# Performance work log

Measured on AMD Instinct MI355X. Metric: run time of the kernel, lower is better.

Reference implementation:

```python
import jax, jax.numpy as jnp
import numpy as np

N_EMBD = 1024
N_HEAD = 16
HEAD_DIM = N_EMBD // N_HEAD


def setup_inputs() -> dict:
    key = jax.random.key(0)
    ks = jax.random.split(key, 5)
    B, S = 2, 2048
    scale = 0.02
    return {
        "hidden_states": jax.random.normal(ks[0], (B, S, N_EMBD), dtype=jnp.float32),
        "w_attn": jax.random.normal(ks[1], (N_EMBD, 3 * N_EMBD), dtype=jnp.float32) * scale,
        "b_attn": jnp.zeros((3 * N_EMBD,), dtype=jnp.float32),
        "w_proj": jax.random.normal(ks[2], (N_EMBD, N_EMBD), dtype=jnp.float32) * scale,
        "b_proj": jnp.zeros((N_EMBD,), dtype=jnp.float32),
    }


def reference(hidden_states, w_attn, b_attn, w_proj, b_proj):
    B, S, _ = hidden_states.shape
    qkv = hidden_states @ w_attn + b_attn                     # [B,S,3E]
    q, k, v = jnp.split(qkv, 3, axis=-1)                      # each [B,S,E]

    def split_heads(t):  # [B,S,E] -> [B,H,S,D]
        return t.reshape(B, S, N_HEAD, HEAD_DIM).transpose(0, 2, 1, 3)

    q, k, v = split_heads(q), split_heads(k), split_heads(v)

    scores = jnp.einsum("bhqd,bhkd->bhqk", q, k) / np.sqrt(HEAD_DIM).astype(np.float32)
    causal = jnp.tril(jnp.ones((S, S), dtype=bool))
    scores = jnp.where(causal[None, None], scores, jnp.float32(-jnp.inf))
    attn = jax.nn.softmax(scores, axis=-1)                    # [B,H,S,S]
    out = jnp.einsum("bhqk,bhkd->bhqd", attn, v)              # [B,H,S,D]
    out = out.transpose(0, 2, 1, 3).reshape(B, S, N_EMBD)     # merge heads
    out = out @ w_proj + b_proj
    return out
```

## Files before the change

kernel.cpp:

```cpp
#include <hip/hip_runtime.h>
#include <hip/hip_bf16.h>


typedef __attribute__((ext_vector_type(4))) float  float4v;
typedef __attribute__((ext_vector_type(8))) short  short8v;
typedef __attribute__((ext_vector_type(4))) short  short4v;

#define ATT_SCALE 0.18033688011112042f

__device__ __forceinline__ short f2bf(float f) {
  union { float f; unsigned u; } v; v.f = f;
  unsigned r = v.u + 0x7fffu + ((v.u >> 16) & 1u);
  return (short)(r >> 16);
}
__device__ __forceinline__ float bf2f(short s) {
  union { unsigned u; float f; } v; v.u = ((unsigned)(unsigned short)s) << 16;
  return v.f;
}

__device__ __forceinline__ short4v pack_bf16x4(float a, float b, float c, float d) {
  unsigned x0 = __builtin_bit_cast(unsigned, a) + 0x8000u;
  unsigned x1 = __builtin_bit_cast(unsigned, b) + 0x8000u;
  unsigned x2 = __builtin_bit_cast(unsigned, c) + 0x8000u;
  unsigned x3 = __builtin_bit_cast(unsigned, d) + 0x8000u;
  union { unsigned u[2]; short4v s; } r;
  r.u[0] = __builtin_amdgcn_perm(x1, x0, 0x07060302);
  r.u[1] = __builtin_amdgcn_perm(x3, x2, 0x07060302);
  return r.s;
}

__device__ __forceinline__ short4v cvt_pk_bf16x4(float a, float b, float c, float d) {
  union { unsigned u[2]; short4v s; } r;
  asm("v_cvt_pk_bf16_f32 %0, %1, %2" : "=v"(r.u[0]) : "v"(a), "v"(b));
  asm("v_cvt_pk_bf16_f32 %0, %1, %2" : "=v"(r.u[1]) : "v"(c), "v"(d));
  return r.s;
}

__device__ __forceinline__ void gl_lds16(const void* g, void* l) {
  __builtin_amdgcn_global_load_lds(
      (const __attribute__((address_space(1))) unsigned*)g,
      (__attribute__((address_space(3))) unsigned*)l, 16, 0, 0);
}

__global__ __launch_bounds__(256) void prep_kernel(
    const float* __restrict__ hidden, const float* __restrict__ w_attn,
    const float* __restrict__ w_proj, short* __restrict__ hA,
    short* __restrict__ wqkvT, short* __restrict__ wprojT) {
  __shared__ float tile[32][33];
  const int bx = blockIdx.x, t = threadIdx.x;
  if (bx < 4096) {
    const size_t i = ((size_t)bx * 256 + t) * 4;
    float4v v = *(const float4v*)(hidden + i);
    short4v o;
    #pragma unroll
    for (int k = 0; k < 4; k++) o[k] = f2bf(v[k]);
    *(short4v*)(hA + i) = o;
    return;
  }
  const float* in; short* out; int R, C, cx, cy;
  if (bx < 4096 + 3072) {
    in = w_attn; out = wqkvT; R = 1024; C = 3072;
    cx = (bx - 4096) % 96; cy = (bx - 4096) / 96;
  } else {
    in = w_proj; out = wprojT; R = 1024; C = 1024;
    cx = (bx - 7168) % 32; cy = (bx - 7168) / 32;
  }
  const int tx = t & 31, ty = t >> 5;
  const int c0 = cx * 32, r0 = cy * 32;
  #pragma unroll
  for (int i = 0; i < 4; i++)
    tile[ty + i * 8][tx] = in[(size_t)(r0 + ty + i * 8) * C + c0 + tx];
  __syncthreads();
  #pragma unroll
  for (int i = 0; i < 4; i++) {
    const int cc = ty + i * 8;
    out[(size_t)(c0 + cc) * R + r0 + tx] = f2bf(tile[tx][cc]);
  }
}

template<int RB, int MODE>
__global__ __launch_bounds__(256) void gemm_bt(
    const short* __restrict__ A, const short* __restrict__ Bt,
    const float* __restrict__ bias, void* __restrict__ Cout,
    short* __restrict__ vA, int M, int N, int K)
{
  __shared__ short As[2][RB][32];
  __shared__ short Bs[2][128][32];
  const int MI = RB / 32;
  const int t    = threadIdx.x;
  const int lane = t & 63;
  const int wave = t >> 6;
  const int wm   = (wave >> 1) * (RB / 2);
  const int wn   = (wave & 1) * 64;
  const int l16  = lane & 15;
  const int quad = lane >> 4;
  const int row0 = blockIdx.y * RB;
  const int col0 = blockIdx.x * 128;

  float4v acc[MI][4] = {};

  const int srow = lane >> 2;
  const int scol = (lane & 3) * 8;
  const int gcol = ((lane & 3) ^ ((srow >> 1) & 3)) * 8;
  const int rquad = (quad ^ ((l16 >> 1) & 3)) * 8;

  const short* gA0 = A + (size_t)(row0 + wave * ((RB == 128) ? 32 : 16) + srow) * K + gcol;
  const short* gA1 = gA0 + (size_t)16 * K;
  const short* gB0 = Bt + (size_t)(col0 + wave * 32 + srow) * K + gcol;
  const short* gB1 = gB0 + (size_t)16 * K;

  const int NI = K / 32;
  {
    if (RB == 128) {
      gl_lds16(gA0, &As[0][wave * 32 + srow][scol]);
      gl_lds16(gA1, &As[0][wave * 32 + 16 + srow][scol]);
    } else {
      gl_lds16(gA0, &As[0][(wave * 16 + srow) & (RB - 1)][scol]);
    }
    gl_lds16(gB0, &Bs[0][wave * 32 + srow][scol]);
    gl_lds16(gB1, &Bs[0][wave * 32 + 16 + srow][scol]);
  }

  for (int i = 0; i < NI; i++) {
    const int buf = i & 1;
    __syncthreads();
    if (i + 1 < NI) {
      const int k1 = (i + 1) * 32;
      if (RB == 128) {
        gl_lds16(gA0 + k1, &As[buf ^ 1][wave * 32 + srow][scol]);
        gl_lds16(gA1 + k1, &As[buf ^ 1][wave * 32 + 16 + srow][scol]);
      } else {
        gl_lds16(gA0 + k1, &As[buf ^ 1][(wave * 16 + srow) & (RB - 1)][scol]);
      }
      gl_lds16(gB0 + k1, &Bs[buf ^ 1][wave * 32 + srow][scol]);
      gl_lds16(gB1 + k1, &Bs[buf ^ 1][wave * 32 + 16 + srow][scol]);
    }
    short8v af[MI], bf[4];
    #pragma unroll
    for (int ii = 0; ii < MI; ii++)
      af[ii] = *(const short8v*)&As[buf][wm + ii * 16 + l16][rquad];
    #pragma unroll
    for (int j = 0; j < 4; j++)
      bf[j] = *(const short8v*)&Bs[buf][wn + j * 16 + l16][rquad];
    #pragma unroll
    for (int ii = 0; ii < MI; ii++)
      #pragma unroll
      for (int j = 0; j < 4; j++)
        acc[ii][j] = __builtin_amdgcn_mfma_f32_16x16x32_bf16(af[ii], bf[j], acc[ii][j], 0, 0, 0);
  }

  if (MODE == 2 && col0 >= 2048) {
    const int b  = row0 >> 11;
    const int hh = ((col0 - 2048) >> 6) + (wn >> 6);
    const int kt = ((row0 & 2047) >> 6) + (wm >> 6);
    short* vbase = vA + ((size_t)((b * 16 + hh) * 32 + kt) * 8) * 512;
    #pragma unroll
    for (int j = 0; j < 4; j++) {
      const float bv = bias[col0 + wn + j * 16 + l16];
      #pragma unroll
      for (int kwp = 0; kwp < 2; kwp++) {
        short8v s8;
        #pragma unroll
        for (int kw = 0; kw < 2; kw++) {
          short4v q4 = pack_bf16x4(acc[kwp * 2 + kw][j][0] + bv,
                                   acc[kwp * 2 + kw][j][1] + bv,
                                   acc[kwp * 2 + kw][j][2] + bv,
                                   acc[kwp * 2 + kw][j][3] + bv);
          #pragma unroll
          for (int r = 0; r < 4; r++) s8[kw * 4 + r] = q4[r];
        }
        *(short8v*)(vbase + ((size_t)(kwp * 4 + j) * 64 + lane) * 8) = s8;
      }
    }
    return;
  }

  #pragma unroll
  for (int j = 0; j < 4; j++) {
    const int col = col0 + wn + j * 16 + l16;
    const float sc = (MODE == 2 && col < 1024) ? ATT_SCALE : 1.0f;
    const float bv = bias[col];
    #pragma unroll
    for (int i = 0; i < MI; i++) {
      #pragma unroll
      for (int r = 0; r < 4; r++) {
        const int row = row0 + wm + i * 16 + quad * 4 + r;
        const float v = (acc[i][j][r] + bv) * sc;
        if (MODE == 2) ((short*)Cout)[(size_t)row * N + col] = f2bf(v);
        else           ((float*)Cout)[(size_t)row * N + col] = v;
      }
    }
  }
}

__global__ __launch_bounds__(256, 2) void attn_mfma(
    const short* __restrict__ qkv, const short* __restrict__ vA,
    short* __restrict__ P0, short* __restrict__ P1, float* __restrict__ lp)
{
  __shared__ short KA[2][8 * 512];

  const int bh = blockIdx.y;
  const int b = bh >> 4, h = bh & 15;
  const int s = 79 - blockIdx.x;
  int qt = 0, sbase = 0;
  for (;;) { const int nc = (qt >> 3) + 1; if (s < sbase + nc) break; sbase += nc; qt++; }
  const int c = s - sbase;
  const int kt0  = c * 8;
  const int kend = min(qt + 1, kt0 + 8);

  const int t = threadIdx.x;
  const int lane = t & 63, w = t >> 6;
  const int l16 = lane & 15, quad = lane >> 4;

  const size_t base = (size_t)b * 2048 * 3072;
  const int qoff = h * 64, koff = 1024 + h * 64;
  const int qg = qt * 64 + w * 16 + l16;

  short8v qf[2];
  #pragma unroll
  for (int ks = 0; ks < 2; ks++)
    qf[ks] = *(const short8v*)(qkv + base + (size_t)qg * 3072 + qoff + ks * 32 + quad * 8);

  float4v O[4] = {};
  float l = 0.0f;

  const int id0 = w * 2, id1 = id0 + 1;
  const int jm0 = id0 & 3, ks0 = id0 >> 2;
  const int jm1 = id1 & 3, ks1 = id1 >> 2;
  const short* kg0 = qkv + base + (size_t)(jm0 * 16 + l16) * 3072 + koff + ks0 * 32 + quad * 8;
  const short* kg1 = qkv + base + (size_t)(jm1 * 16 + l16) * 3072 + koff + ks1 * 32 + quad * 8;
  const short* vg  = vA + (size_t)(bh * 32) * 4096 + lane * 8;

  gl_lds16(kg0 + (size_t)kt0 * 64 * 3072, &KA[0][id0 * 512 + lane * 8]);
  gl_lds16(kg1 + (size_t)kt0 * 64 * 3072, &KA[0][id1 * 512 + lane * 8]);

  for (int kt = kt0; kt < kend; kt++) {
    const int buf = (kt - kt0) & 1;
    __syncthreads();

    short8v vv[8];
    #pragma unroll
    for (int id = 0; id < 8; id++)
      vv[id] = *(const short8v*)(vg + (size_t)kt * 4096 + id * 512);

    if (kt + 1 < kend) {
      gl_lds16(kg0 + (size_t)(kt + 1) * 64 * 3072, &KA[buf ^ 1][id0 * 512 + lane * 8]);
      gl_lds16(kg1 + (size_t)(kt + 1) * 64 * 3072, &KA[buf ^ 1][id1 * 512 + lane * 8]);
    }

    float4v sv[4] = {};
    __builtin_amdgcn_s_setprio(1);
    #pragma unroll
    for (int ks = 0; ks < 2; ks++)
      #pragma unroll
      for (int jm = 0; jm < 4; jm++) {
        const short8v kf = *(const short8v*)&KA[buf][(ks * 4 + jm) * 512 + lane * 8];
        sv[jm] = __builtin_amdgcn_mfma_f32_16x16x32_bf16(kf, qf[ks], sv[jm], 0, 0, 0);
      }
    __builtin_amdgcn_s_setprio(0);

    if (kt == qt) {
      #pragma unroll
      for (int jm = 0; jm < 4; jm++) {
        const int kv = kt * 64 + jm * 16 + quad * 4;
        #pragma unroll
        for (int r = 0; r < 4; r++)
          if (kv + r > qg) sv[jm][r] = -INFINITY;
      }
    }

    short4v pk[4];
    #pragma unroll
    for (int jm = 0; jm < 4; jm++) {
      float p0 = __builtin_amdgcn_exp2f(sv[jm][0]);
      float p1 = __builtin_amdgcn_exp2f(sv[jm][1]);
      float p2 = __builtin_amdgcn_exp2f(sv[jm][2]);
      float p3 = __builtin_amdgcn_exp2f(sv[jm][3]);
      l += (p0 + p1) + (p2 + p3);
      pk[jm] = cvt_pk_bf16x4(p0, p1, p2, p3);
    }

    __builtin_amdgcn_s_setprio(1);
    #pragma unroll
    for (int id = 0; id < 8; id++) {
      const int kwp = id >> 2, dm = id & 3;
      const short8v v8 = vv[id];
      const short4v v0 = {v8[0], v8[1], v8[2], v8[3]};
      const short4v v1 = {v8[4], v8[5], v8[6], v8[7]};
      O[dm] = __builtin_amdgcn_mfma_f32_16x16x16bf16_1k(v0, pk[kwp * 2],     O[dm], 0, 0, 0);
      O[dm] = __builtin_amdgcn_mfma_f32_16x16x16bf16_1k(v1, pk[kwp * 2 + 1], O[dm], 0, 0, 0);
    }
    __builtin_amdgcn_s_setprio(0);
  }

  l += __shfl_xor(l, 16);
  l += __shfl_xor(l, 32);
  const int i = bh * 80 + s;
  short* pp = (i < 2048) ? (P0 + (size_t)i * 4096) : (P1 + (size_t)(i - 2048) * 4096);
  const int row = w * 16 + l16;
  if (quad == 0) lp[(size_t)i * 64 + row] = l;
  short* pr = pp + row * 64;
  #pragma unroll
  for (int dm = 0; dm < 4; dm++)
    *(short4v*)(pr + dm * 16 + quad * 4) =
        pack_bf16x4(O[dm][0], O[dm][1], O[dm][2], O[dm][3]);
}

__global__ __launch_bounds__(256) void merge_attn(
    const short* __restrict__ P0, const short* __restrict__ P1,
    const float* __restrict__ lp, short* __restrict__ aout)
{
  const int idx = blockIdx.x * 256 + threadIdx.x;
  const int q = idx >> 7;
  const int rest = idx & 127;
  const int h  = rest >> 3;
  const int dg = (rest & 7) * 8;
  const int b  = q >> 11;
  const int qr = q & 2047;
  const int qt = qr >> 6;
  const int row = qr & 63;
  const int a = qt >> 3, bq = qt & 7;
  const int off = qt + 4 * a * (a - 1) + a * bq;
  const int nc  = a + 1;
  const int bh  = b * 16 + h;

  float acc[8] = {};
  float suml = 0.0f;
  for (int c = 0; c < nc; c++) {
    const int i = bh * 80 + off + c;
    const short* pp = (i < 2048) ? (P0 + (size_t)i * 4096) : (P1 + (size_t)(i - 2048) * 4096);
    const short8v o = *(const short8v*)(pp + row * 64 + dg);
    #pragma unroll
    for (int k = 0; k < 8; k++) acc[k] += bf2f(o[k]);
    suml += lp[(size_t)i * 64 + row];
  }
  const float inv = 1.0f / suml;
  short8v ov;
  #pragma unroll
  for (int k = 0; k < 8; k++) ov[k] = f2bf(acc[k] * inv);
  *(short8v*)(aout + (size_t)q * 1024 + h * 64 + dg) = ov;
}

extern "C" void kernel_launch(void* const* d_in, const int* in_sizes, int n_in,
                              void* d_out, int out_size, void* d_ws, size_t ws_size,
                              hipStream_t stream) {
  const float* hidden = (const float*)d_in[0];
  const float* w_attn = (const float*)d_in[1];
  const float* b_attn = (const float*)d_in[2];
  const float* w_proj = (const float*)d_in[3];
  const float* b_proj = (const float*)d_in[4];
  float* outp = (float*)d_out;

  char* ws = (char*)d_ws;
  short* hA     = (short*)(ws);
  float* lp     = (float*)(ws + 8ull  * 1024 * 1024);
  short* wqkvT  = (short*)(ws + 8ull  * 1024 * 1024);
  short* wprojT = (short*)(ws + 14ull * 1024 * 1024);
  short* qkvb   = (short*)(ws + 16ull * 1024 * 1024);
  short* vAbuf  = (short*)(ws + 40ull * 1024 * 1024);
  short* aout   = (short*)(ws + 40ull * 1024 * 1024);
  short* P0     = (short*)d_out;

  prep_kernel<<<8192, 256, 0, stream>>>(hidden, w_attn, w_proj, hA, wqkvT, wprojT);
  gemm_bt<128, 2><<<dim3(24, 32), 256, 0, stream>>>(hA, wqkvT, b_attn, qkvb, vAbuf, 4096, 3072, 1024);
  attn_mfma<<<dim3(80, 32), 256, 0, stream>>>(qkvb, vAbuf, P0, hA, lp);
  merge_attn<<<2048, 256, 0, stream>>>(P0, hA, lp, aout);
  gemm_bt<64, 0><<<dim3(8, 64), 256, 0, stream>>>(aout, wprojT, b_proj, outp, nullptr, 4096, 1024, 1024);
}
```

Baseline: 203.7 us.

## Triple-buffer GEMM LDS staging with explicit vmcnt waits and single barrier

Moves the bf16 GEMM main loop from double-buffered to triple-buffered LDS, prefetching two K-tiles ahead. __syncthreads is replaced by explicit s_waitcnt vmcnt counts plus a raw s_barrier, so outstanding global-to-LDS loads for the next-next tile can stay in flight across the barrier. This aims to hide more global memory latency. In exchange LDS use per block grows by half, which may lower occupancy, and the hand-written vmcnt counts must match the number of loads issued per stage.

```diff
diff --git a/kernel.cpp b/kernel.cpp
--- a/kernel.cpp
+++ b/kernel.cpp
@@ -84,8 +84,8 @@
     const float* __restrict__ bias, void* __restrict__ Cout,
     short* __restrict__ vA, int M, int N, int K)
 {
-  __shared__ short As[2][RB][32];
-  __shared__ short Bs[2][128][32];
+  __shared__ short As[3][RB][32];
+  __shared__ short Bs[3][128][32];
   const int MI = RB / 32;
   const int t    = threadIdx.x;
   const int lane = t & 63;
@@ -110,31 +110,30 @@
   const short* gB1 = gB0 + (size_t)16 * K;
 
   const int NI = K / 32;
-  {
+
+  auto stage = [&](int kt, int b) {
+    const int k0 = kt * 32;
     if (RB == 128) {
-      gl_lds16(gA0, &As[0][wave * 32 + srow][scol]);
-      gl_lds16(gA1, &As[0][wave * 32 + 16 + srow][scol]);
+      gl_lds16(gA0 + k0, &As[b][wave * 32 + srow][scol]);
+      gl_lds16(gA1 + k0, &As[b][wave * 32 + 16 + srow][scol]);
     } else {
-      gl_lds16(gA0, &As[0][(wave * 16 + srow) & (RB - 1)][scol]);
-    }
-    gl_lds16(gB0, &Bs[0][wave * 32 + srow][scol]);
-    gl_lds16(gB1, &Bs[0][wave * 32 + 16 + srow][scol]);
-  }
-
+      gl_lds16(gA0 + k0, &As[b][(wave * 16 + srow) & (RB - 1)][scol]);
+    }
+    gl_lds16(gB0 + k0, &Bs[b][wave * 32 + srow][scol]);
+    gl_lds16(gB1 + k0, &Bs[b][wave * 32 + 16 + srow][scol]);
+  };
+
+  stage(0, 0);
+  stage(1, 1);
+  if (RB == 128) asm volatile("s_waitcnt vmcnt(4)" ::: "memory");
+  else           asm volatile("s_waitcnt vmcnt(3)" ::: "memory");
+  __builtin_amdgcn_s_barrier();
+  __builtin_amdgcn_sched_barrier(0);
+
+  int buf = 0;
   for (int i = 0; i < NI; i++) {
-    const int buf = i & 1;
-    __syncthreads();
-    if (i + 1 < NI) {
-      const int k1 = (i + 1) * 32;
-      if (RB == 128) {
-        gl_lds16(gA0 + k1, &As[buf ^ 1][wave * 32 + srow][scol]);
-        gl_lds16(gA1 + k1, &As[buf ^ 1][wave * 32 + 16 + srow][scol]);
-      } else {
-        gl_lds16(gA0 + k1, &As[buf ^ 1][(wave * 16 + srow) & (RB - 1)][scol]);
-      }
-      gl_lds16(gB0 + k1, &Bs[buf ^ 1][wave * 32 + srow][scol]);
-      gl_lds16(gB1 + k1, &Bs[buf ^ 1][wave * 32 + 16 + srow][scol]);
-    }
+    if (i + 2 < NI) stage(i + 2, (buf + 2 >= 3) ? buf - 1 : buf + 2);
+
     short8v af[MI], bf[4];
     #pragma unroll
     for (int ii = 0; ii < MI; ii++)
@@ -147,6 +146,18 @@
       #pragma unroll
       for (int j = 0; j < 4; j++)
         acc[ii][j] = __builtin_amdgcn_mfma_f32_16x16x32_bf16(af[ii], bf[j], acc[ii][j], 0, 0, 0);
+
+    if (i + 1 < NI) {
+      if (i + 2 < NI) {
+        if (RB == 128) asm volatile("s_waitcnt vmcnt(4)" ::: "memory");
+        else           asm volatile("s_waitcnt vmcnt(3)" ::: "memory");
+      } else {
+        asm volatile("s_waitcnt vmcnt(0)" ::: "memory");
+      }
+      __builtin_amdgcn_s_barrier();
+      __builtin_amdgcn_sched_barrier(0);
+    }
+    buf = (buf >= 2) ? 0 : buf + 1;
   }
 
   if (MODE == 2 && col0 >= 2048) {
```

New measurement: 206.1 us. No clear change (+1.2%).
